# Kernel tuning notes

Hardware: AMD Instinct MI355X
Metric: run time of the kernel (lower is better)

The kernel has to match this reference:

```python
import jax, jax.numpy as jnp
import numpy as np

FEAT_STRIDE = 32.0
ANGLE_THRESH = 15.0           # cfg.TRAIN.FCGN.ANGLE_THRESH
NEG_POS_RATIO = 3             # cfg.TRAIN.FCGN.NEG_POS_RATIO
EPS = 1e-14                   # cfg.EPS
BBOX_INSIDE_WEIGHT = 1.0      # cfg.TRAIN.FCGN.BBOX_INSIDE_WEIGHTS[0]
MEANS = np.array([0., 0., 0., 0., 0.], np.float32)   # cfg.FCGN.BBOX_NORMALIZE_MEANS
STDS = np.array([0.1, 0.1, 0.2, 0.2, 0.1], np.float32)  # cfg.FCGN.BBOX_NORMALIZE_STDS
BS, K, N = 32, 50000, 32


def grasp_encode(loc, priors):
    # loc, priors: [bs, K, 5] = (x, y, w, h, angle)
    xy = (loc[..., 0:2] - priors[..., 0:2]) / priors[..., 2:4]
    wh = jnp.log(loc[..., 2:4] / priors[..., 2:4])
    ang = loc[..., 4:5] - priors[..., 4:5]
    return jnp.concatenate([xy, wh, ang], axis=-1)


def setup_inputs() -> dict:
    key = jax.random.key(0)
    k1, k2, k3 = jax.random.split(key, 3)
    conf = jax.random.normal(k1, (BS, K, 2), jnp.float32)
    u = jax.random.uniform(k2, (BS, N, 5), jnp.float32)
    gt = jnp.concatenate([u[..., 0:2] * 608.0,
                          10.0 + 50.0 * u[..., 2:4],
                          (u[..., 4:5] - 0.5) * 180.0], axis=-1)
    v = jax.random.uniform(k3, (BS, K, 5), jnp.float32)
    priors = jnp.concatenate([v[..., 0:2] * 608.0,
                              10.0 + 50.0 * v[..., 2:4],
                              (v[..., 4:5] - 0.5) * 180.0], axis=-1)
    return {"conf": conf, "gt": gt, "priors": priors}


def reference(conf, gt, priors):
    bs, num_priors, _ = priors.shape
    xthresh = FEAT_STRIDE / 2
    ythresh = FEAT_STRIDE / 2

    # ---- anchor-prior matching (ANGLE_MATCH branch) ----
    # valid gt rows: not all-zero padding. [bs, N]
    mask_gt = jnp.sum(gt == 0, axis=2) != gt.shape[2]
    # broadcast compares: [bs, K, N]
    xdiff = jnp.abs(priors[:, :, 0:1] - gt[:, None, :, 0])
    ydiff = jnp.abs(priors[:, :, 1:2] - gt[:, None, :, 1])
    angdiff = jnp.abs(priors[:, :, 4:5] - gt[:, None, :, 4])
    match = ((xdiff <= xthresh) & (ydiff <= ythresh)
             & (angdiff <= ANGLE_THRESH) & mask_gt[:, None, :])

    match_num = jnp.sum(match, axis=2)                      # [bs, K] int
    label = (match_num > 0).astype(jnp.int32)               # [bs, K]

    # sum-and-normalize matched gts per prior (scatter-style reduce)
    matchf = match.astype(gt.dtype)
    loc = jnp.einsum('bkn,bnd->bkd', matchf, gt) + EPS      # [bs, K, 5]
    denom = jnp.maximum(match_num, 1).astype(gt.dtype)[..., None]
    loc = jnp.where((match_num > 0)[..., None], loc / denom, loc)
    loc_t = grasp_encode(loc, priors)                       # [bs, K, 5]

    # ---- hard-negative mining (uses conf.data -> stop_gradient) ----
    c = jax.lax.stop_gradient(conf)                         # [bs, K, 2]
    lse = jax.nn.logsumexp(c, axis=2)                       # [bs, K]
    gathered = jnp.take_along_axis(c, label[..., None], axis=2)[..., 0]
    loss_c = lse - gathered                                 # [bs, K]
    pos = label > 0
    loss_c = jnp.where(pos, -1.0, loss_c)
    # double-sort rank trick
    loss_idx = jnp.argsort(-loss_c, axis=1)                 # descending
    idx_rank = jnp.argsort(loss_idx, axis=1)                # rank of each prior
    num_pos = jnp.sum(pos.astype(jnp.int32), axis=1, keepdims=True)  # [bs, 1]
    num_neg = NEG_POS_RATIO * num_pos
    neg = (idx_rank < num_neg) & (~pos)

    conf_t = jnp.where((~neg) & (~pos), -1, label)          # ignore = -1

    iw = (pos.astype(jnp.float32) * BBOX_INSIDE_WEIGHT)[..., None]
    iw = jnp.broadcast_to(iw, (bs, num_priors, 5))
    # BBOX_POSITIVE_WEIGHTS < 0 branch: ow = (pos|neg) / ((num_pos+num_neg) | 1)
    ow_denom = jnp.bitwise_or(num_pos + num_neg, 1).astype(jnp.float32)
    ow = ((pos | neg).astype(jnp.float32) / ow_denom)[..., None]
    ow = jnp.broadcast_to(ow, (bs, num_priors, 5))

    # ---- precomputed bbox normalization ----
    loc_t = (loc_t - jnp.asarray(MEANS)) / jnp.asarray(STDS)
    return loc_t, conf_t, iw, ow
```

## Files before the change

### kernel.cpp

```cpp
#include <hip/hip_runtime.h>
#include <cstdint>

#define BS 32
#define K 50000
#define K4 12500
#define NCH 49
#define NGT 32
#define KROW (K * 5)
#define KEY_NEG1 0x407FFFFFu

__device__ __forceinline__ unsigned f2key(float f) {
    unsigned b = __float_as_uint(f);
    return (b & 0x80000000u) ? ~b : (b | 0x80000000u);
}

struct Sel { int bin; int want; int ceq; };

__device__ __forceinline__ void pick256(const unsigned* __restrict__ hist_row,
                                        int want, int tid, int* T, Sel* r) {
    int h = 0;
    if (tid < 256) { h = (int)hist_row[tid]; T[tid] = h; }
    __syncthreads();
#pragma unroll
    for (int o = 1; o < 256; o <<= 1) {
        int add = 0;
        if (tid < 256) add = (tid + o < 256) ? T[tid + o] : 0;
        __syncthreads();
        if (tid < 256) T[tid] += add;
        __syncthreads();
    }
    if (tid < 256) {
        const int Ti = T[tid];
        const int Tn = (tid == 255) ? (want - 1) : T[tid + 1];
        if (Ti >= want && Tn < want) { r->bin = tid; r->ceq = h; r->want = want - (Ti - h); }
    }
    __syncthreads();
}

__device__ __forceinline__ int want_of(int np) {
    const long long w0 = 3LL * (long long)np;
    return (w0 > K) ? K : (int)w0;
}

__global__ __launch_bounds__(256) void kA(const float* __restrict__ conf,
                                          const float* __restrict__ gt,
                                          const float* __restrict__ priors,
                                          float* __restrict__ loc_t,
                                          unsigned* __restrict__ keys,
                                          unsigned* __restrict__ ghist,
                                          int* __restrict__ numpos) {
    const int b    = blockIdx.y;
    const int tid  = threadIdx.x;
    const int k0   = blockIdx.x * 1024;
    const int lane = tid & 63;
    const int rep  = tid & 7;

    __shared__ float sb[5120];
    __shared__ float sg[NGT * 5];
    __shared__ int   lh[8][256];
    __shared__ int   lpos;

    if (tid == 0) lpos = 0;
    if (tid < NGT * 5) sg[tid] = gt[b * NGT * 5 + tid];
#pragma unroll
    for (int r2 = 0; r2 < 8; r2++) lh[r2][tid] = 0;

    const int ebase = k0 * 5;
    const int rem   = KROW - ebase;
    const int nf4   = (rem < 5120 ? rem : 5120) >> 2;
    const float4* p4 = (const float4*)(priors + (size_t)b * KROW + ebase);
#pragma unroll
    for (int j = 0; j < 5; j++) {
        const int i4 = j * 256 + tid;
        if (i4 < nf4) ((float4*)sb)[i4] = p4[i4];
    }
    __syncthreads();

    float px[4], py[4], pw[4], ph[4], pa[4];
#pragma unroll
    for (int c = 0; c < 4; c++) {
        const int l = (c * 256 + tid) * 5;
        px[c] = sb[l];     py[c] = sb[l + 1]; pw[c] = sb[l + 2];
        ph[c] = sb[l + 3]; pa[c] = sb[l + 4];
    }
    __syncthreads();

    const unsigned* gtu = (const unsigned*)(gt + (size_t)b * NGT * 5);
    unsigned mask[4] = {0u, 0u, 0u, 0u};
#pragma unroll
    for (int n = 0; n < NGT; n++) {
        const unsigned ux = gtu[n * 5],     uy = gtu[n * 5 + 1],
                       uw = gtu[n * 5 + 2], uh = gtu[n * 5 + 3],
                       ua = gtu[n * 5 + 4];
        const bool gvalid = ((ux | uy | uw | uh | ua) != 0u);
        const float gx = gvalid ? __uint_as_float(ux) : 1e30f;
        const float gy = __uint_as_float(uy);
        const float ga = __uint_as_float(ua);
#pragma unroll
        for (int c = 0; c < 4; c++) {
            const bool m = (fabsf(px[c] - gx) <= 16.f) &
                           (fabsf(py[c] - gy) <= 16.f) &
                           (fabsf(pa[c] - ga) <= 15.f);
            mask[c] |= m ? (1u << n) : 0u;
        }
    }

    const float2* c2p = (const float2*)conf + (size_t)b * K;
#pragma unroll
    for (int c = 0; c < 4; c++) {
        const int k = k0 + c * 256 + tid;
        const bool vk = (k < K);
        const int cnt = __popc(mask[c]);
        float sx = 0.f, sy = 0.f, sw = 0.f, sh = 0.f, sa = 0.f;
        unsigned mm = mask[c];
        while (__any(mm != 0u)) {
            if (mm) {
                const int n = __ffs(mm) - 1;
                mm &= mm - 1u;
                const int base = n * 5;
                sx += sg[base];     sy += sg[base + 1]; sw += sg[base + 2];
                sh += sg[base + 3]; sa += sg[base + 4];
            }
        }
        const float inv = 1.0f / fmaxf((float)cnt, 1.0f);
        const float rpw = 1.0f / pw[c], rph = 1.0f / ph[c];
        const float lx  = (sx + 1e-14f) * inv;
        const float ly  = (sy + 1e-14f) * inv;
        const float lw  = (sw + 1e-14f) * inv;
        const float lh2 = (sh + 1e-14f) * inv;
        const float la  = (sa + 1e-14f) * inv;
        const int l = (c * 256 + tid) * 5;
        sb[l]     = (lx - px[c]) * rpw * (1.0f / 0.1f);
        sb[l + 1] = (ly - py[c]) * rph * (1.0f / 0.1f);
        sb[l + 2] = __logf(lw * rpw) * (1.0f / 0.2f);
        sb[l + 3] = __logf(lh2 * rph) * (1.0f / 0.2f);
        sb[l + 4] = (la - pa[c]) * (1.0f / 0.1f);
        if (vk) {
            const float2 cc = c2p[k];
            const float mmx = fmaxf(cc.x, cc.y);
            const float lse = mmx + __logf(__expf(cc.x - mmx) + __expf(cc.y - mmx));
            const float loss = (cnt > 0) ? -1.0f : (lse - cc.x);
            const unsigned key = f2key(loss);
            keys[(size_t)b * K + k] = key;
            atomicAdd(&lh[rep][key >> 24], 1);
        }
        const unsigned long long pm = __ballot(vk && (cnt > 0));
        if (lane == 0 && pm) atomicAdd(&lpos, (int)__popcll(pm));
    }
    __syncthreads();

    float4* o4 = (float4*)(loc_t + (size_t)b * KROW + ebase);
#pragma unroll
    for (int j = 0; j < 5; j++) {
        const int i4 = j * 256 + tid;
        if (i4 < nf4) o4[i4] = ((const float4*)sb)[i4];
    }
    int s = 0;
#pragma unroll
    for (int r2 = 0; r2 < 8; r2++) s += lh[r2][tid];
    if (s) atomicAdd(&ghist[b * 256 + tid], (unsigned)s);
    if (tid == 0 && lpos) atomicAdd(&numpos[b], lpos);
}

__global__ __launch_bounds__(1024) void kSel(const unsigned* __restrict__ keys,
                                             const unsigned* __restrict__ ghist,
                                             const int* __restrict__ numpos,
                                             unsigned* __restrict__ thresh,
                                             unsigned* __restrict__ tieflag,
                                             float* __restrict__ confo) {
    const int row = blockIdx.x, tid = threadIdx.x;
    const int np = numpos[row];
    if (np <= 0) {
        if (tid == 0) { thresh[row] = 0xFFFFFFFFu; tieflag[row] = 0u; }
        return;
    }
    __shared__ int T[256];
    __shared__ Sel r;
    __shared__ int lh[4][256];
    __shared__ unsigned lhm[256];

    pick256(ghist + row * 256, want_of(np), tid, T, &r);
    unsigned pfx = (unsigned)r.bin;

    const uint4* kr4 = (const uint4*)(keys + (size_t)row * K);
#pragma unroll
    for (int level = 2; level >= 0; level--) {
        const int shift = level * 8;
        ((int*)lh)[tid] = 0;
        __syncthreads();
        for (int i = tid; i < K4; i += 1024) {
            const uint4 kv = kr4[i];
            const unsigned ka[4] = {kv.x, kv.y, kv.z, kv.w};
#pragma unroll
            for (int j = 0; j < 4; j++)
                if ((ka[j] >> (shift + 8)) == pfx)
                    atomicAdd(&lh[tid & 3][(ka[j] >> shift) & 255u], 1);
        }
        __syncthreads();
        if (tid < 256)
            lhm[tid] = (unsigned)(lh[0][tid] + lh[1][tid] + lh[2][tid] + lh[3][tid]);
        __syncthreads();
        pick256(lhm, r.want, tid, T, &r);
        pfx = (pfx << 8) | (unsigned)r.bin;
    }

    const unsigned uT = pfx;
    const int bud = r.want;
    const bool tie = (r.want < r.ceq);
    if (tid == 0) { thresh[row] = uT; tieflag[row] = tie ? 1u : 0u; }
    if (!tie) return;

    __shared__ int wsum[16];
    __shared__ int s_run;
    if (tid == 0) s_run = 0;
    __syncthreads();
    const unsigned* kr = keys + (size_t)row * K;
    float* co = confo + (size_t)row * K;
    for (int base = 0; base < K; base += 1024) {
        const int i = base + tid;
        const unsigned key = (i < K) ? kr[i] : 0u;
        const bool eq = (i < K) && (key == uT);
        const unsigned long long bal = __ballot(eq);
        const int lane = tid & 63, wid = tid >> 6;
        if (lane == 0) wsum[wid] = __popcll(bal);
        __syncthreads();
        if (tid == 0) {
            int acc = s_run;
            for (int w = 0; w < 16; w++) { const int t = wsum[w]; wsum[w] = acc; acc += t; }
            s_run = acc;
        }
        __syncthreads();
        if (i < K) {
            const int rank = wsum[wid] + __popcll(bal & ((1ull << lane) - 1ull));
            const bool pos = (key == KEY_NEG1);
            const bool sel = (key > uT) || (eq && rank < bud);
            co[i] = pos ? 1.0f : ((sel && !pos) ? 0.0f : -1.0f);
        }
        __syncthreads();
    }
}

__global__ __launch_bounds__(256) void kD12(const unsigned* __restrict__ keys,
                                            const unsigned* __restrict__ thresh,
                                            const unsigned* __restrict__ tieflag,
                                            const int* __restrict__ numpos,
                                            float* __restrict__ confo,
                                            float* __restrict__ iw,
                                            float* __restrict__ ow) {
    const int tid = threadIdx.x;
    const int g0 = blockIdx.x * 256;
    const int g = g0 + tid;
    __shared__ float si[1280];
    __shared__ float so2[1280];
    const int row = g / K;
    const unsigned key = keys[g];
    float c;
    if (tieflag[row]) {
        c = __uint_as_float(key);
    } else {
        const unsigned uT = thresh[row];
        const bool pos = (key == KEY_NEG1);
        c = pos ? 1.0f : ((key >= uT) ? 0.0f : -1.0f);
        confo[g] = c;
    }
    const float inv = 1.0f / (float)((numpos[row] * 4) | 1);
    const float iwv = (c == 1.0f) ? 1.0f : 0.0f;
    const float owv = (c >= 0.0f) ? inv : 0.0f;
#pragma unroll
    for (int j = 0; j < 5; j++) { si[tid * 5 + j] = iwv; so2[tid * 5 + j] = owv; }
    __syncthreads();
    const size_t e0 = (size_t)g0 * 5;
#pragma unroll
    for (int j = 0; j < 5; j++) {
        const int s = j * 256 + tid;
        iw[e0 + s] = si[s];
        ow[e0 + s] = so2[s];
    }
}

extern "C" void kernel_launch(void* const* d_in, const int* in_sizes, int n_in,
                              void* d_out, int out_size, void* d_ws, size_t ws_size,
                              hipStream_t stream) {
    const float* conf   = (const float*)d_in[0];
    const float* gt     = (const float*)d_in[1];
    const float* priors = (const float*)d_in[2];

    float* out   = (float*)d_out;
    float* loc_t = out;
    float* confo = out + 8000000;
    float* iw    = out + 9600000;
    float* ow    = out + 17600000;

    unsigned* keys  = (unsigned*)confo;
    int*      numpos  = (int*)d_ws;
    unsigned* thresh  = (unsigned*)d_ws + 32;
    unsigned* tieflag = (unsigned*)d_ws + 64;
    unsigned* ghist   = (unsigned*)d_ws + 96;

    hipMemsetAsync(d_ws, 0, (96 + 8192) * sizeof(int), stream);

    dim3 gA(NCH, BS);
    kA<<<gA, 256, 0, stream>>>(conf, gt, priors, loc_t, keys, ghist, numpos);
    kSel<<<BS, 1024, 0, stream>>>(keys, ghist, numpos, thresh, tieflag, confo);
    kD12<<<(BS * K) / 256, 256, 0, stream>>>(keys, thresh, tieflag, numpos,
                                             confo, iw, ow);
}
```

Baseline: 73.23 us.

## Give each thread four contiguous priors and drop LDS staging in kA and kD12

kA now has each thread load its four consecutive priors (20 floats) and conf pairs directly from global memory with float4 loads. It writes loc_t and keys back as float4/uint4, removing the shared-memory staging buffer and its barriers. kD12 does the same, handling four elements per thread and writing iw/ow/confo with vector stores instead of going through LDS. This removes LDS traffic and syncs, at the cost of more registers per thread, strided per-thread accesses (20-float stride) that may coalesce less well, and a grid four times smaller for kD12.

```diff
diff --git a/kernel.cpp b/kernel.cpp
--- a/kernel.cpp
+++ b/kernel.cpp
@@ -51,39 +51,32 @@
                                           int* __restrict__ numpos) {
     const int b    = blockIdx.y;
     const int tid  = threadIdx.x;
-    const int k0   = blockIdx.x * 1024;
+    const int k4   = blockIdx.x * 1024 + tid * 4;
     const int lane = tid & 63;
     const int rep  = tid & 7;
 
-    __shared__ float sb[5120];
     __shared__ float sg[NGT * 5];
     __shared__ int   lh[8][256];
     __shared__ int   lpos;
 
+    if (tid < NGT * 5) sg[tid] = gt[b * NGT * 5 + tid];
+#pragma unroll
+    for (int r2 = 0; r2 < 8; r2++) lh[r2][tid] = 0;
     if (tid == 0) lpos = 0;
-    if (tid < NGT * 5) sg[tid] = gt[b * NGT * 5 + tid];
-#pragma unroll
-    for (int r2 = 0; r2 < 8; r2++) lh[r2][tid] = 0;
-
-    const int ebase = k0 * 5;
-    const int rem   = KROW - ebase;
-    const int nf4   = (rem < 5120 ? rem : 5120) >> 2;
-    const float4* p4 = (const float4*)(priors + (size_t)b * KROW + ebase);
-#pragma unroll
-    for (int j = 0; j < 5; j++) {
-        const int i4 = j * 256 + tid;
-        if (i4 < nf4) ((float4*)sb)[i4] = p4[i4];
-    }
-    __syncthreads();
-
-    float px[4], py[4], pw[4], ph[4], pa[4];
-#pragma unroll
-    for (int c = 0; c < 4; c++) {
-        const int l = (c * 256 + tid) * 5;
-        px[c] = sb[l];     py[c] = sb[l + 1]; pw[c] = sb[l + 2];
-        ph[c] = sb[l + 3]; pa[c] = sb[l + 4];
-    }
-    __syncthreads();
+    __syncthreads();
+
+    const bool vk = (k4 < K);
+
+    float p[20];
+    float cf[8];
+    if (vk) {
+        const float4* pp = (const float4*)(priors + (size_t)b * KROW + (size_t)k4 * 5);
+#pragma unroll
+        for (int j = 0; j < 5; j++) ((float4*)p)[j] = pp[j];
+        const float4* cp = (const float4*)(conf + ((size_t)b * K + k4) * 2);
+        ((float4*)cf)[0] = cp[0];
+        ((float4*)cf)[1] = cp[1];
+    }
 
     const unsigned* gtu = (const unsigned*)(gt + (size_t)b * NGT * 5);
     unsigned mask[4] = {0u, 0u, 0u, 0u};
@@ -98,18 +91,17 @@
         const float ga = __uint_as_float(ua);
 #pragma unroll
         for (int c = 0; c < 4; c++) {
-            const bool m = (fabsf(px[c] - gx) <= 16.f) &
-                           (fabsf(py[c] - gy) <= 16.f) &
-                           (fabsf(pa[c] - ga) <= 15.f);
+            const bool m = (fabsf(p[c * 5]     - gx) <= 16.f) &
+                           (fabsf(p[c * 5 + 1] - gy) <= 16.f) &
+                           (fabsf(p[c * 5 + 4] - ga) <= 15.f);
             mask[c] |= m ? (1u << n) : 0u;
         }
     }
 
-    const float2* c2p = (const float2*)conf + (size_t)b * K;
+    unsigned keyv[4];
+    int npos = 0;
 #pragma unroll
     for (int c = 0; c < 4; c++) {
-        const int k = k0 + c * 256 + tid;
-        const bool vk = (k < K);
         const int cnt = __popc(mask[c]);
         float sx = 0.f, sy = 0.f, sw = 0.f, sh = 0.f, sa = 0.f;
         unsigned mm = mask[c];
@@ -122,39 +114,47 @@
                 sh += sg[base + 3]; sa += sg[base + 4];
             }
         }
+        const float px = p[c * 5],     py = p[c * 5 + 1], pw = p[c * 5 + 2],
+                    ph = p[c * 5 + 3], pa = p[c * 5 + 4];
         const float inv = 1.0f / fmaxf((float)cnt, 1.0f);
-        const float rpw = 1.0f / pw[c], rph = 1.0f / ph[c];
+        const float rpw = 1.0f / pw, rph = 1.0f / ph;
         const float lx  = (sx + 1e-14f) * inv;
         const float ly  = (sy + 1e-14f) * inv;
         const float lw  = (sw + 1e-14f) * inv;
         const float lh2 = (sh + 1e-14f) * inv;
         const float la  = (sa + 1e-14f) * inv;
-        const int l = (c * 256 + tid) * 5;
-        sb[l]     = (lx - px[c]) * rpw * (1.0f / 0.1f);
-        sb[l + 1] = (ly - py[c]) * rph * (1.0f / 0.1f);
-        sb[l + 2] = __logf(lw * rpw) * (1.0f / 0.2f);
-        sb[l + 3] = __logf(lh2 * rph) * (1.0f / 0.2f);
-        sb[l + 4] = (la - pa[c]) * (1.0f / 0.1f);
-        if (vk) {
-            const float2 cc = c2p[k];
-            const float mmx = fmaxf(cc.x, cc.y);
-            const float lse = mmx + __logf(__expf(cc.x - mmx) + __expf(cc.y - mmx));
-            const float loss = (cnt > 0) ? -1.0f : (lse - cc.x);
-            const unsigned key = f2key(loss);
-            keys[(size_t)b * K + k] = key;
-            atomicAdd(&lh[rep][key >> 24], 1);
-        }
-        const unsigned long long pm = __ballot(vk && (cnt > 0));
-        if (lane == 0 && pm) atomicAdd(&lpos, (int)__popcll(pm));
-    }
-    __syncthreads();
-
-    float4* o4 = (float4*)(loc_t + (size_t)b * KROW + ebase);
-#pragma unroll
-    for (int j = 0; j < 5; j++) {
-        const int i4 = j * 256 + tid;
-        if (i4 < nf4) o4[i4] = ((const float4*)sb)[i4];
-    }
+        p[c * 5]     = (lx - px) * rpw * (1.0f / 0.1f);
+        p[c * 5 + 1] = (ly - py) * rph * (1.0f / 0.1f);
+        p[c * 5 + 2] = __logf(lw * rpw) * (1.0f / 0.2f);
+        p[c * 5 + 3] = __logf(lh2 * rph) * (1.0f / 0.2f);
+        p[c * 5 + 4] = (la - pa) * (1.0f / 0.1f);
+
+        const float c0 = cf[c * 2], c1 = cf[c * 2 + 1];
+        const float mmx = fmaxf(c0, c1);
+        const float lse = mmx + __logf(__expf(c0 - mmx) + __expf(c1 - mmx));
+        const float loss = (cnt > 0) ? -1.0f : (lse - c0);
+        keyv[c] = f2key(loss);
+        npos += (cnt > 0) ? 1 : 0;
+        if (vk) atomicAdd(&lh[rep][keyv[c] >> 24], 1);
+    }
+
+    if (vk) {
+        *(uint4*)(keys + (size_t)b * K + k4) =
+            make_uint4(keyv[0], keyv[1], keyv[2], keyv[3]);
+        float4* o4 = (float4*)(loc_t + (size_t)b * KROW + (size_t)k4 * 5);
+#pragma unroll
+        for (int j = 0; j < 5; j++) o4[j] = ((const float4*)p)[j];
+    }
+
+    int wsum = 0;
+#pragma unroll
+    for (int bit = 0; bit < 3; bit++) {
+        const unsigned long long bm = __ballot(vk && ((npos >> bit) & 1));
+        wsum += __popcll(bm) << bit;
+    }
+    if (lane == 0 && wsum) atomicAdd(&lpos, wsum);
+    __syncthreads();
+
     int s = 0;
 #pragma unroll
     for (int r2 = 0; r2 < 8; r2++) s += lh[r2][tid];
@@ -247,34 +247,36 @@
                                             float* __restrict__ confo,
                                             float* __restrict__ iw,
                                             float* __restrict__ ow) {
-    const int tid = threadIdx.x;
-    const int g0 = blockIdx.x * 256;
-    const int g = g0 + tid;
-    __shared__ float si[1280];
-    __shared__ float so2[1280];
-    const int row = g / K;
-    const unsigned key = keys[g];
-    float c;
-    if (tieflag[row]) {
-        c = __uint_as_float(key);
-    } else {
-        const unsigned uT = thresh[row];
-        const bool pos = (key == KEY_NEG1);
-        c = pos ? 1.0f : ((key >= uT) ? 0.0f : -1.0f);
-        confo[g] = c;
-    }
+    const int t = blockIdx.x * 256 + threadIdx.x;
+    const int g4 = t * 4;
+    if (g4 >= BS * K) return;
+    const int row = g4 / K;
+    const uint4 kv = *(const uint4*)(keys + g4);
+    const unsigned ka[4] = {kv.x, kv.y, kv.z, kv.w};
+    const unsigned uT = thresh[row];
+    const unsigned tf = tieflag[row];
     const float inv = 1.0f / (float)((numpos[row] * 4) | 1);
-    const float iwv = (c == 1.0f) ? 1.0f : 0.0f;
-    const float owv = (c >= 0.0f) ? inv : 0.0f;
-#pragma unroll
-    for (int j = 0; j < 5; j++) { si[tid * 5 + j] = iwv; so2[tid * 5 + j] = owv; }
-    __syncthreads();
-    const size_t e0 = (size_t)g0 * 5;
+    float c[4], iwv[20], owv[20];
+#pragma unroll
+    for (int j = 0; j < 4; j++) {
+        if (tf) {
+            c[j] = __uint_as_float(ka[j]);
+        } else {
+            const bool pos = (ka[j] == KEY_NEG1);
+            c[j] = pos ? 1.0f : ((ka[j] >= uT) ? 0.0f : -1.0f);
+        }
+        const float iv = (c[j] == 1.0f) ? 1.0f : 0.0f;
+        const float ov = (c[j] >= 0.0f) ? inv : 0.0f;
+#pragma unroll
+        for (int e = 0; e < 5; e++) { iwv[j * 5 + e] = iv; owv[j * 5 + e] = ov; }
+    }
+    if (!tf) *(float4*)(confo + g4) = make_float4(c[0], c[1], c[2], c[3]);
+    float4* i4 = (float4*)(iw + (size_t)g4 * 5);
+    float4* o4 = (float4*)(ow + (size_t)g4 * 5);
 #pragma unroll
     for (int j = 0; j < 5; j++) {
-        const int s = j * 256 + tid;
-        iw[e0 + s] = si[s];
-        ow[e0 + s] = so2[s];
+        i4[j] = ((const float4*)iwv)[j];
+        o4[j] = ((const float4*)owv)[j];
     }
 }
 
@@ -291,7 +293,7 @@
     float* iw    = out + 9600000;
     float* ow    = out + 17600000;
 
-    unsigned* keys  = (unsigned*)confo;
+    unsigned* keys = (unsigned*)confo;
     int*      numpos  = (int*)d_ws;
     unsigned* thresh  = (unsigned*)d_ws + 32;
     unsigned* tieflag = (unsigned*)d_ws + 64;
@@ -302,6 +304,6 @@
     dim3 gA(NCH, BS);
     kA<<<gA, 256, 0, stream>>>(conf, gt, priors, loc_t, keys, ghist, numpos);
     kSel<<<BS, 1024, 0, stream>>>(keys, ghist, numpos, thresh, tieflag, confo);
-    kD12<<<(BS * K) / 256, 256, 0, stream>>>(keys, thresh, tieflag, numpos,
-                                             confo, iw, ow);
-}
+    kD12<<<(BS * K / 4 + 255) / 256, 256, 0, stream>>>(keys, thresh, tieflag,
+                                                       numpos, confo, iw, ow);
+}
```

New measurement: 90.15 us. +23.1%, slower.

## Replace global histogram atomics with per-block partials reduced in selection kernel

Applied to the files above, without the earlier changes.

The first kernel now writes per-block 256-bin histograms and positive counts into scratch space carved from the ow output buffer, instead of doing global atomics. The selection kernel sums these partials itself, which removes the memset launch and the global atomic contention. The conf loads are also hoisted ahead of the matching loop so their latency overlaps the compare work. In exchange, the selection kernel reads 49 partial rows per batch, and the scratch relies on ow being overwritten later by the final kernel.

```diff
diff --git a/kernel.cpp b/kernel.cpp
--- a/kernel.cpp
+++ b/kernel.cpp
@@ -47,8 +47,8 @@
                                           const float* __restrict__ priors,
                                           float* __restrict__ loc_t,
                                           unsigned* __restrict__ keys,
-                                          unsigned* __restrict__ ghist,
-                                          int* __restrict__ numpos) {
+                                          unsigned* __restrict__ ghist_part,
+                                          unsigned* __restrict__ npos_part) {
     const int b    = blockIdx.y;
     const int tid  = threadIdx.x;
     const int k0   = blockIdx.x * 1024;
@@ -84,6 +84,14 @@
         ph[c] = sb[l + 3]; pa[c] = sb[l + 4];
     }
     __syncthreads();
+
+    const float2* c2p = (const float2*)conf + (size_t)b * K;
+    float2 cf[4];
+#pragma unroll
+    for (int c = 0; c < 4; c++) {
+        const int kk = k0 + c * 256 + tid;
+        cf[c] = c2p[kk < K ? kk : K - 1];
+    }
 
     const unsigned* gtu = (const unsigned*)(gt + (size_t)b * NGT * 5);
     unsigned mask[4] = {0u, 0u, 0u, 0u};
@@ -105,7 +113,6 @@
         }
     }
 
-    const float2* c2p = (const float2*)conf + (size_t)b * K;
 #pragma unroll
     for (int c = 0; c < 4; c++) {
         const int k = k0 + c * 256 + tid;
@@ -136,7 +143,7 @@
         sb[l + 3] = __logf(lh2 * rph) * (1.0f / 0.2f);
         sb[l + 4] = (la - pa[c]) * (1.0f / 0.1f);
         if (vk) {
-            const float2 cc = c2p[k];
+            const float2 cc = cf[c];
             const float mmx = fmaxf(cc.x, cc.y);
             const float lse = mmx + __logf(__expf(cc.x - mmx) + __expf(cc.y - mmx));
             const float loss = (cnt > 0) ? -1.0f : (lse - cc.x);
@@ -158,28 +165,42 @@
     int s = 0;
 #pragma unroll
     for (int r2 = 0; r2 < 8; r2++) s += lh[r2][tid];
-    if (s) atomicAdd(&ghist[b * 256 + tid], (unsigned)s);
-    if (tid == 0 && lpos) atomicAdd(&numpos[b], lpos);
+    ghist_part[((size_t)b * NCH + blockIdx.x) * 256 + tid] = (unsigned)s;
+    if (tid == 0) npos_part[b * NCH + blockIdx.x] = (unsigned)lpos;
 }
 
 __global__ __launch_bounds__(1024) void kSel(const unsigned* __restrict__ keys,
-                                             const unsigned* __restrict__ ghist,
-                                             const int* __restrict__ numpos,
+                                             const unsigned* __restrict__ ghist_part,
+                                             const unsigned* __restrict__ npos_part,
+                                             int* __restrict__ numpos,
                                              unsigned* __restrict__ thresh,
                                              unsigned* __restrict__ tieflag,
                                              float* __restrict__ confo) {
     const int row = blockIdx.x, tid = threadIdx.x;
-    const int np = numpos[row];
-    if (np <= 0) {
-        if (tid == 0) { thresh[row] = 0xFFFFFFFFu; tieflag[row] = 0u; }
-        return;
-    }
     __shared__ int T[256];
     __shared__ Sel r;
     __shared__ int lh[4][256];
     __shared__ unsigned lhm[256];
-
-    pick256(ghist + row * 256, want_of(np), tid, T, &r);
+    __shared__ int s_np;
+
+    if (tid == 0) s_np = 0;
+    __syncthreads();
+    if (tid < NCH) atomicAdd(&s_np, (int)npos_part[row * NCH + tid]);
+    if (tid < 256) {
+        unsigned acc = 0;
+        for (int c = 0; c < NCH; c++)
+            acc += ghist_part[((size_t)row * NCH + c) * 256 + tid];
+        lhm[tid] = acc;
+    }
+    __syncthreads();
+    const int np = s_np;
+    if (tid == 0) numpos[row] = np;
+    if (np <= 0) {
+        if (tid == 0) { thresh[row] = 0xFFFFFFFFu; tieflag[row] = 0u; }
+        return;
+    }
+
+    pick256(lhm, want_of(np), tid, T, &r);
     unsigned pfx = (unsigned)r.bin;
 
     const uint4* kr4 = (const uint4*)(keys + (size_t)row * K);
@@ -291,17 +312,19 @@
     float* iw    = out + 9600000;
     float* ow    = out + 17600000;
 
-    unsigned* keys  = (unsigned*)confo;
+    unsigned* keys = (unsigned*)confo;
+    unsigned* owu        = (unsigned*)ow;
+    unsigned* ghist_part = owu;
+    unsigned* npos_part  = owu + 401408;
     int*      numpos  = (int*)d_ws;
     unsigned* thresh  = (unsigned*)d_ws + 32;
     unsigned* tieflag = (unsigned*)d_ws + 64;
-    unsigned* ghist   = (unsigned*)d_ws + 96;
-
-    hipMemsetAsync(d_ws, 0, (96 + 8192) * sizeof(int), stream);
 
     dim3 gA(NCH, BS);
-    kA<<<gA, 256, 0, stream>>>(conf, gt, priors, loc_t, keys, ghist, numpos);
-    kSel<<<BS, 1024, 0, stream>>>(keys, ghist, numpos, thresh, tieflag, confo);
+    kA<<<gA, 256, 0, stream>>>(conf, gt, priors, loc_t, keys,
+                               ghist_part, npos_part);
+    kSel<<<BS, 1024, 0, stream>>>(keys, ghist_part, npos_part, numpos,
+                                  thresh, tieflag, confo);
     kD12<<<(BS * K) / 256, 256, 0, stream>>>(keys, thresh, tieflag, numpos,
                                              confo, iw, ow);
 }
```

New measurement: 66.12 us, median of 2. 9.7% less time.
